# Performance work log

Hardware: AMD Instinct MI355X
Metric: run time of the kernel (lower is better)

Reference implementation:

```python
import jax, jax.numpy as jnp
import numpy as np

VOCAB, E, HID, HD, S, T = 50000, 1024, 1024, 512, 4096, 20
START, STOP, NEG = 18, 19, -10000.0


def setup_inputs() -> dict:
    key = jax.random.key(0)
    ks = jax.random.split(key, 16)
    scale = 0.05
    trans = jax.random.normal(ks[12], (T, T), jnp.float32)
    trans = trans.at[START, :].set(NEG).at[:, START].set(NEG)
    return {
        'sentence': jax.random.randint(ks[0], (S,), 0, VOCAB),
        'embed_table': jax.random.normal(ks[1], (VOCAB, E), jnp.float32) * scale,
        'w_ih_f': jax.random.normal(ks[2], (4 * HD, E), jnp.float32) * scale,
        'w_hh_f': jax.random.normal(ks[3], (4 * HD, HD), jnp.float32) * scale,
        'b_ih_f': jax.random.normal(ks[4], (4 * HD,), jnp.float32) * scale,
        'b_hh_f': jax.random.normal(ks[5], (4 * HD,), jnp.float32) * scale,
        'w_ih_b': jax.random.normal(ks[6], (4 * HD, E), jnp.float32) * scale,
        'w_hh_b': jax.random.normal(ks[7], (4 * HD, HD), jnp.float32) * scale,
        'b_ih_b': jax.random.normal(ks[8], (4 * HD,), jnp.float32) * scale,
        'b_hh_b': jax.random.normal(ks[9], (4 * HD,), jnp.float32) * scale,
        'w_out': jax.random.normal(ks[10], (T, HID), jnp.float32) * scale,
        'b_out': jax.random.normal(ks[11], (T,), jnp.float32) * scale,
        'transitions': trans,
        'h0': jax.random.normal(ks[13], (2, HD), jnp.float32),
        'c0': jax.random.normal(ks[14], (2, HD), jnp.float32),
    }


def _lstm_dir(pre, w_hh, b_hh, h0, c0, reverse):
    # pre: [S, 4HD] = x @ W_ih^T + b_ih (precomputed big GEMM)
    def step(carry, p):
        h, c = carry
        g = p + h @ w_hh.T + b_hh
        i, f, gg, o = jnp.split(g, 4, axis=-1)  # torch gate order i,f,g,o
        c = jax.nn.sigmoid(f) * c + jax.nn.sigmoid(i) * jnp.tanh(gg)
        h = jax.nn.sigmoid(o) * jnp.tanh(c)
        return (h, c), h
    _, hs = jax.lax.scan(step, (h0, c0), pre, reverse=reverse)
    return hs  # [S, HD], time-aligned in both directions


def _get_feats(sentence, embed_table, w_ih_f, w_hh_f, b_ih_f, b_hh_f,
               w_ih_b, w_hh_b, b_ih_b, b_hh_b, w_out, b_out, h0, c0):
    x = embed_table[sentence]                       # [S, E]
    hf = _lstm_dir(x @ w_ih_f.T + b_ih_f, w_hh_f, b_hh_f, h0[0], c0[0], False)
    hb = _lstm_dir(x @ w_ih_b.T + b_ih_b, w_hh_b, b_hh_b, h0[1], c0[1], True)
    lstm_out = jnp.concatenate([hf, hb], axis=-1)   # [S, HID]
    return lstm_out @ w_out.T + b_out               # [S, T]


def reference(sentence, embed_table, w_ih_f, w_hh_f, b_ih_f, b_hh_f,
              w_ih_b, w_hh_b, b_ih_b, b_hh_b, w_out, b_out,
              transitions, h0, c0):
    feats = _get_feats(sentence, embed_table, w_ih_f, w_hh_f, b_ih_f, b_hh_f,
                       w_ih_b, w_hh_b, b_ih_b, b_hh_b, w_out, b_out, h0, c0)
    # Viterbi decode
    init_v = jnp.full((T,), NEG, jnp.float32).at[START].set(0.0)

    def step(fv, feat):
        nt = fv[None, :] + transitions            # [T_cur, T_prev]
        best = jnp.argmax(nt, axis=1)             # backpointers [T]
        fv_new = jnp.max(nt, axis=1) + feat
        return fv_new, best

    fv_last, bptrs = jax.lax.scan(step, init_v, feats)
    terminal = fv_last + transitions[STOP]
    path_score = jnp.max(terminal)
    best_tag = jnp.argmax(terminal)

    def back(tag, bp):
        return bp[tag], tag
    _, path = jax.lax.scan(back, best_tag, bptrs, reverse=True)  # [S]
    return path_score, path
```

## Files before the change

### kernel.cpp

```cpp
#include <hip/hip_runtime.h>
#include <math.h>

#define S_LEN 4096
#define NTAG 20
#define TAG_STOP 19
#define NEGV -10000.0f
#define NWG 16


__global__ void init_ws(unsigned long long* hpub) {
    int i = blockIdx.x * 256 + threadIdx.x;
    if (i < 2048) hpub[i] = 0ull;
}

__device__ __forceinline__ float sigm(float x) { return 1.0f / (1.0f + expf(-x)); }

__launch_bounds__(256)
__global__ void pre_gemm(const int* __restrict__ sent, const float* __restrict__ embed,
                         const float* __restrict__ wf, const float* __restrict__ wb,
                         const float* __restrict__ bihf, const float* __restrict__ bhhf,
                         const float* __restrict__ bihb, const float* __restrict__ bhhb,
                         float* __restrict__ pre)
{
    __shared__ float As[16][68];
    __shared__ float Bs[16][136];
    __shared__ int   srow[64];
    const int tid = threadIdx.x;
    const int bm = blockIdx.x & 63;
    const int bn = blockIdx.x >> 6;
    const int pos0 = bm * 64, row0 = bn * 128;
    if (tid < 64) srow[tid] = sent[pos0 + tid];
    __syncthreads();

    const int tx = tid & 15, ty = tid >> 4;
    float acc[4][8];
    #pragma unroll
    for (int m = 0; m < 4; ++m)
        #pragma unroll
        for (int n = 0; n < 8; ++n) acc[m][n] = 0.f;

    for (int kt = 0; kt < 1024; kt += 16) {
        {
            int m = tid >> 2, kc = (tid & 3) * 4;
            const float* src = embed + (size_t)srow[m] * 1024 + kt + kc;
            float4 v = *(const float4*)src;
            As[kc+0][m] = v.x; As[kc+1][m] = v.y; As[kc+2][m] = v.z; As[kc+3][m] = v.w;
        }
        #pragma unroll
        for (int it = 0; it < 2; ++it) {
            int n = (tid >> 2) + it * 64;
            int kc = (tid & 3) * 4;
            int grow = row0 + n;
            const float* wsrc = (grow < 2048) ? (wf + (size_t)grow * 1024)
                                              : (wb + (size_t)(grow - 2048) * 1024);
            float4 v = *(const float4*)(wsrc + kt + kc);
            Bs[kc+0][n] = v.x; Bs[kc+1][n] = v.y; Bs[kc+2][n] = v.z; Bs[kc+3][n] = v.w;
        }
        __syncthreads();
        #pragma unroll
        for (int kk = 0; kk < 16; ++kk) {
            float a[4], b[8];
            float4 av = *(const float4*)&As[kk][ty * 4];
            a[0] = av.x; a[1] = av.y; a[2] = av.z; a[3] = av.w;
            float4 bv0 = *(const float4*)&Bs[kk][tx * 8];
            float4 bv1 = *(const float4*)&Bs[kk][tx * 8 + 4];
            b[0]=bv0.x; b[1]=bv0.y; b[2]=bv0.z; b[3]=bv0.w;
            b[4]=bv1.x; b[5]=bv1.y; b[6]=bv1.z; b[7]=bv1.w;
            #pragma unroll
            for (int m = 0; m < 4; ++m)
                #pragma unroll
                for (int n = 0; n < 8; ++n) acc[m][n] += a[m] * b[n];
        }
        __syncthreads();
    }
    #pragma unroll
    for (int m = 0; m < 4; ++m) {
        int pos = pos0 + ty * 4 + m;
        #pragma unroll
        for (int n = 0; n < 8; ++n) {
            int grow = row0 + tx * 8 + n;
            float bias = (grow < 2048) ? (bihf[grow] + bhhf[grow])
                                       : (bihb[grow - 2048] + bhhb[grow - 2048]);
            pre[(size_t)pos * 4096 + grow] = acc[m][n] + bias;
        }
    }
}

template<int P>
__device__ __forceinline__ void lstm_step(
    int s, int dir, int wg, int j, int ks, int su, bool own, int sidx, bool gate,
    const float* __restrict__ pre, const float* __restrict__ h0,
    float* __restrict__ hs, unsigned long long* pub,
    float (&buf)[2][576],
    const float (&wr0)[32], const float (&wr1)[32],
    const float (&wr2)[32], const float (&wr3)[32],
    float (&pf)[4], float& c_reg)
{
    if (s == 0) {
        buf[0][sidx] = h0[dir * 512 + su];
    } else if (!own) {
        const unsigned int expect = (unsigned int)s;
        unsigned long long u = __hip_atomic_load(&pub[P * 512 + su],
                                                 __ATOMIC_RELAXED, __HIP_MEMORY_SCOPE_AGENT);
        while ((unsigned int)(u >> 32) < expect)
            u = __hip_atomic_load(&pub[P * 512 + su],
                                  __ATOMIC_RELAXED, __HIP_MEMORY_SCOPE_AGENT);
        buf[P][sidx] = __uint_as_float((unsigned int)u);
    }
    __syncthreads();

    float a0 = 0.f, a1 = 0.f, a2 = 0.f, a3 = 0.f;
    const float* hp = &buf[P][ks * 36];
    #pragma unroll
    for (int q = 0; q < 8; ++q) {
        float4 h4 = ((const float4*)hp)[q];
        a0 += wr0[q*4+0]*h4.x + wr0[q*4+1]*h4.y + wr0[q*4+2]*h4.z + wr0[q*4+3]*h4.w;
        a1 += wr1[q*4+0]*h4.x + wr1[q*4+1]*h4.y + wr1[q*4+2]*h4.z + wr1[q*4+3]*h4.w;
        a2 += wr2[q*4+0]*h4.x + wr2[q*4+1]*h4.y + wr2[q*4+2]*h4.z + wr2[q*4+3]*h4.w;
        a3 += wr3[q*4+0]*h4.x + wr3[q*4+1]*h4.y + wr3[q*4+2]*h4.z + wr3[q*4+3]*h4.w;
    }
    a0 += __shfl_xor(a0, 1); a0 += __shfl_xor(a0, 2); a0 += __shfl_xor(a0, 4); a0 += __shfl_xor(a0, 8);
    a1 += __shfl_xor(a1, 1); a1 += __shfl_xor(a1, 2); a1 += __shfl_xor(a1, 4); a1 += __shfl_xor(a1, 8);
    a2 += __shfl_xor(a2, 1); a2 += __shfl_xor(a2, 2); a2 += __shfl_xor(a2, 4); a2 += __shfl_xor(a2, 8);
    a3 += __shfl_xor(a3, 1); a3 += __shfl_xor(a3, 2); a3 += __shfl_xor(a3, 4); a3 += __shfl_xor(a3, 8);

    if (gate) {
        float gi = a0 + pf[0], gf = a1 + pf[1], gg = a2 + pf[2], go = a3 + pf[3];
        float cn = sigm(gf) * c_reg + sigm(gi) * tanhf(gg);
        float hN = sigm(go) * tanhf(cn);
        c_reg = cn;
        const int pos = dir ? (S_LEN - 1 - s) : s;
        hs[((size_t)dir * S_LEN + pos) * 512 + j] = hN;
        buf[P ^ 1][j + 4 * wg] = hN;
        unsigned long long uv = ((unsigned long long)(unsigned int)(s + 1) << 32)
                              | (unsigned long long)__float_as_uint(hN);
        __hip_atomic_store(&pub[(P ^ 1) * 512 + j], uv,
                           __ATOMIC_RELAXED, __HIP_MEMORY_SCOPE_AGENT);
        if (s + 2 < S_LEN) {
            const int pp = dir ? (S_LEN - 3 - s) : (s + 2);
            const float* pb = pre + (size_t)pp * 4096 + dir * 2048 + j;
            pf[0] = pb[0]; pf[1] = pb[512]; pf[2] = pb[1024]; pf[3] = pb[1536];
        }
    }
}

__launch_bounds__(512, 2)
__global__ void lstm_kernel(const float* __restrict__ pre,
                            const float* __restrict__ w_hh_f, const float* __restrict__ w_hh_b,
                            const float* __restrict__ h0, const float* __restrict__ c0,
                            float* __restrict__ hs, unsigned long long* __restrict__ h_pub)
{
    const int dir  = blockIdx.x >> 4;
    const int wg   = blockIdx.x & 15;
    const int tid  = threadIdx.x;
    const int wv   = tid >> 6;
    const int lane = tid & 63;
    const int rg   = lane >> 4;
    const int ks   = lane & 15;
    const int j    = wg * 32 + wv * 4 + rg;
    const float* w_hh = dir ? w_hh_b : w_hh_f;

    __shared__ float buf[2][576];

    float wr0[32], wr1[32], wr2[32], wr3[32];
    {
        const float* wbase = w_hh + (size_t)j * 512 + ks * 32;
        #pragma unroll
        for (int q = 0; q < 8; ++q) {
            float4 v0 = *(const float4*)(wbase + 0 * 262144 + q * 4);
            wr0[q*4+0] = v0.x; wr0[q*4+1] = v0.y; wr0[q*4+2] = v0.z; wr0[q*4+3] = v0.w;
            float4 v1 = *(const float4*)(wbase + 1 * 262144 + q * 4);
            wr1[q*4+0] = v1.x; wr1[q*4+1] = v1.y; wr1[q*4+2] = v1.z; wr1[q*4+3] = v1.w;
            float4 v2 = *(const float4*)(wbase + 2 * 262144 + q * 4);
            wr2[q*4+0] = v2.x; wr2[q*4+1] = v2.y; wr2[q*4+2] = v2.z; wr2[q*4+3] = v2.w;
            float4 v3 = *(const float4*)(wbase + 3 * 262144 + q * 4);
            wr3[q*4+0] = v3.x; wr3[q*4+1] = v3.y; wr3[q*4+2] = v3.z; wr3[q*4+3] = v3.w;
        }
    }

    const bool gate = (ks == 0);
    float c_reg = 0.f;
    float pfA[4] = {0,0,0,0}, pfB[4] = {0,0,0,0};
    if (gate) {
        c_reg = c0[dir * 512 + j];
        const int p0 = dir ? (S_LEN - 1) : 0;
        const int p1 = dir ? (S_LEN - 2) : 1;
        const float* b0 = pre + (size_t)p0 * 4096 + dir * 2048 + j;
        const float* b1 = pre + (size_t)p1 * 4096 + dir * 2048 + j;
        pfA[0] = b0[0]; pfA[1] = b0[512]; pfA[2] = b0[1024]; pfA[3] = b0[1536];
        pfB[0] = b1[0]; pfB[1] = b1[512]; pfB[2] = b1[1024]; pfB[3] = b1[1536];
    }

    const int  su   = tid;
    const bool own  = ((su >> 5) == wg);
    const int  sidx = su + ((su >> 5) << 2);
    unsigned long long* pub = h_pub + dir * 1024;

    for (int s = 0; s < S_LEN; s += 2) {
        lstm_step<0>(s,     dir, wg, j, ks, su, own, sidx, gate,
                     pre, h0, hs, pub, buf, wr0, wr1, wr2, wr3, pfA, c_reg);
        lstm_step<1>(s + 1, dir, wg, j, ks, su, own, sidx, gate,
                     pre, h0, hs, pub, buf, wr0, wr1, wr2, wr3, pfB, c_reg);
    }
}

__launch_bounds__(256)
__global__ void feats_kernel(const float* __restrict__ hs, const float* __restrict__ w_out,
                             const float* __restrict__ b_out, float* __restrict__ feats)
{
    const int pos = blockIdx.x;
    const int tid = threadIdx.x;
    __shared__ float hbuf[1024];
    __shared__ float red[160];
    {
        const float* hf = hs + (size_t)pos * 512;
        const float* hb = hs + ((size_t)S_LEN + pos) * 512;
        if (tid < 128) *(float4*)&hbuf[tid * 4]           = *(const float4*)&hf[tid * 4];
        else           *(float4*)&hbuf[512 + (tid-128)*4] = *(const float4*)&hb[(tid - 128) * 4];
    }
    __syncthreads();
    if (tid < 160) {
        int tag = tid >> 3, part = tid & 7;
        const float* wrow = w_out + (size_t)tag * 1024 + part * 128;
        const float* hrow = hbuf + part * 128;
        float sum = 0.f;
        #pragma unroll
        for (int q = 0; q < 32; ++q) {
            float4 a = ((const float4*)hrow)[q];
            float4 b = ((const float4*)wrow)[q];
            sum += a.x*b.x + a.y*b.y + a.z*b.z + a.w*b.w;
        }
        red[tid] = sum;
    }
    __syncthreads();
    if (tid < NTAG) {
        float sum = b_out[tid];
        #pragma unroll
        for (int p = 0; p < 8; ++p) sum += red[tid * 8 + p];
        feats[(size_t)pos * NTAG + tid] = sum;
    }
}

__launch_bounds__(256)
__global__ void viterbi_kernel(const float* __restrict__ feats, const float* __restrict__ trans,
                               unsigned char* __restrict__ bptr, float* __restrict__ out)
{
    __shared__ float feat_lds[64 * NTAG];
    __shared__ int sh_best;
    __shared__ unsigned char Mmap[8][NTAG];
    __shared__ unsigned char entry_s[8];
    const int tid = threadIdx.x;

    if (tid < 64) {
        const int lane = tid;
        const int i = (lane < NTAG) ? lane : (NTAG - 1);
        float trow[NTAG];
        #pragma unroll
        for (int jj = 0; jj < NTAG; ++jj) trow[jj] = trans[i * NTAG + jj];
        float fv[NTAG];
        #pragma unroll
        for (int jj = 0; jj < NTAG; ++jj) fv[jj] = (jj == 18) ? 0.f : NEGV;

        for (int blk = 0; blk < 64; ++blk) {
            #pragma unroll
            for (int q = 0; q < 20; ++q)
                feat_lds[q * 64 + lane] = feats[blk * 1280 + q * 64 + lane];
            for (int ss = 0; ss < 64; ++ss) {
                int s = blk * 64 + ss;
                float best = fv[0] + trow[0];
                int bj = 0;
                #pragma unroll
                for (int jj = 1; jj < NTAG; ++jj) {
                    float cand = fv[jj] + trow[jj];
                    if (cand > best) { best = cand; bj = jj; }
                }
                float fnew = best + feat_lds[ss * NTAG + i];
                if (lane < NTAG) bptr[s * NTAG + lane] = (unsigned char)bj;
                #pragma unroll
                for (int jj = 0; jj < NTAG; ++jj) fv[jj] = __shfl(fnew, jj);
            }
        }
        if (lane == 0) {
            float best = -1e30f; int bt = 0;
            for (int jj = 0; jj < NTAG; ++jj) {
                float t2 = fv[jj] + trans[TAG_STOP * NTAG + jj];
                if (t2 > best) { best = t2; bt = jj; }
            }
            out[0] = best;
            sh_best = bt;
        }
    }
    __syncthreads();
    if (tid < 160) {
        int c = tid / NTAG, e = tid % NTAG;
        int tag = e;
        for (int t = (c + 1) * 512 - 1; t >= c * 512; --t) tag = bptr[t * NTAG + tag];
        Mmap[c][e] = (unsigned char)tag;
    }
    __syncthreads();
    if (tid == 0) {
        int e = sh_best;
        entry_s[7] = (unsigned char)e;
        for (int c = 7; c >= 1; --c) { e = Mmap[c][e]; entry_s[c - 1] = (unsigned char)e; }
    }
    __syncthreads();
    if (tid < 8) {
        int c = tid;
        int tag = entry_s[c];
        out[1 + (c + 1) * 512 - 1] = (float)tag;
        for (int t = (c + 1) * 512 - 1; t > c * 512; --t) {
            tag = bptr[t * NTAG + tag];
            out[1 + t - 1] = (float)tag;
        }
    }
}

extern "C" void kernel_launch(void* const* d_in, const int* in_sizes, int n_in,
                              void* d_out, int out_size, void* d_ws, size_t ws_size,
                              hipStream_t stream) {
    (void)in_sizes; (void)n_in; (void)out_size; (void)ws_size;
    const int*   sent  = (const int*)d_in[0];
    const float* embed = (const float*)d_in[1];
    const float* wihf  = (const float*)d_in[2];
    const float* whhf  = (const float*)d_in[3];
    const float* bihf  = (const float*)d_in[4];
    const float* bhhf  = (const float*)d_in[5];
    const float* wihb  = (const float*)d_in[6];
    const float* whhb  = (const float*)d_in[7];
    const float* bihb  = (const float*)d_in[8];
    const float* bhhb  = (const float*)d_in[9];
    const float* wout  = (const float*)d_in[10];
    const float* bout  = (const float*)d_in[11];
    const float* trans = (const float*)d_in[12];
    const float* h0    = (const float*)d_in[13];
    const float* c0    = (const float*)d_in[14];

    char* ws = (char*)d_ws;
    unsigned long long* h_pub = (unsigned long long*)(ws + 4096);
    float* pre   = (float*)(ws + 65536);
    float* hs    = (float*)(ws + 65536 + (size_t)4096 * 4096 * 4);
    float* feats = (float*)(ws + 65536 + (size_t)4096 * 4096 * 4 + (size_t)2 * 4096 * 512 * 4);
    unsigned char* bptr = (unsigned char*)(feats + (size_t)S_LEN * NTAG);
    float* out = (float*)d_out;

    hipLaunchKernelGGL(init_ws, dim3(8), dim3(256), 0, stream, h_pub);
    hipLaunchKernelGGL(pre_gemm, dim3(2048), dim3(256), 0, stream,
                       sent, embed, wihf, wihb, bihf, bhhf, bihb, bhhb, pre);
    hipLaunchKernelGGL(lstm_kernel, dim3(32), dim3(512), 0, stream,
                       pre, whhf, whhb, h0, c0, hs, h_pub);
    hipLaunchKernelGGL(feats_kernel, dim3(S_LEN), dim3(256), 0, stream,
                       hs, wout, bout, feats);
    hipLaunchKernelGGL(viterbi_kernel, dim3(1), dim3(256), 0, stream,
                       feats, trans, bptr, out);
}
```

Measured before the change: 10.70 ms.

## Split LSTM recurrent gate rows across two half-groups with 1024-thread blocks

The recurrent LSTM kernel now runs 1024 threads per workgroup instead of 512. Each hidden unit is served by 32 lanes, and each 16-lane half computes two of the four gate dot products, cutting per-thread weight registers from 128 to 64 and halving the serial FMA chain per step. The halves exchange partial sums with a shuffle. The gate lane in one half publishes h to global memory while the other half writes hs and the shared buffer, and polling is spread across 8 lanes per unit. The cost is more threads per workgroup and barrier participants, plus an extra cross-half shuffle on each step.

```diff
diff --git a/kernel.cpp b/kernel.cpp
--- a/kernel.cpp
+++ b/kernel.cpp
@@ -5,7 +5,6 @@
 #define NTAG 20
 #define TAG_STOP 19
 #define NEGV -10000.0f
-#define NWG 16
 
 
 __global__ void init_ws(unsigned long long* hpub) {
@@ -88,54 +87,57 @@
 
 template<int P>
 __device__ __forceinline__ void lstm_step(
-    int s, int dir, int wg, int j, int ks, int su, bool own, int sidx, bool gate,
+    int s, int dir, int wg, int j, int hf, int ks,
+    bool isPoller, int p, bool own, int sidx, bool glane,
     const float* __restrict__ pre, const float* __restrict__ h0,
     float* __restrict__ hs, unsigned long long* pub,
     float (&buf)[2][576],
     const float (&wr0)[32], const float (&wr1)[32],
-    const float (&wr2)[32], const float (&wr3)[32],
     float (&pf)[4], float& c_reg)
 {
     if (s == 0) {
-        buf[0][sidx] = h0[dir * 512 + su];
-    } else if (!own) {
+        if (isPoller) buf[0][sidx] = h0[dir * 512 + p];
+    } else if (isPoller && !own) {
         const unsigned int expect = (unsigned int)s;
-        unsigned long long u = __hip_atomic_load(&pub[P * 512 + su],
+        unsigned long long u = __hip_atomic_load(&pub[P * 512 + p],
                                                  __ATOMIC_RELAXED, __HIP_MEMORY_SCOPE_AGENT);
         while ((unsigned int)(u >> 32) < expect)
-            u = __hip_atomic_load(&pub[P * 512 + su],
+            u = __hip_atomic_load(&pub[P * 512 + p],
                                   __ATOMIC_RELAXED, __HIP_MEMORY_SCOPE_AGENT);
         buf[P][sidx] = __uint_as_float((unsigned int)u);
     }
     __syncthreads();
 
-    float a0 = 0.f, a1 = 0.f, a2 = 0.f, a3 = 0.f;
+    float a0 = 0.f, a1 = 0.f;
     const float* hp = &buf[P][ks * 36];
     #pragma unroll
     for (int q = 0; q < 8; ++q) {
         float4 h4 = ((const float4*)hp)[q];
         a0 += wr0[q*4+0]*h4.x + wr0[q*4+1]*h4.y + wr0[q*4+2]*h4.z + wr0[q*4+3]*h4.w;
         a1 += wr1[q*4+0]*h4.x + wr1[q*4+1]*h4.y + wr1[q*4+2]*h4.z + wr1[q*4+3]*h4.w;
-        a2 += wr2[q*4+0]*h4.x + wr2[q*4+1]*h4.y + wr2[q*4+2]*h4.z + wr2[q*4+3]*h4.w;
-        a3 += wr3[q*4+0]*h4.x + wr3[q*4+1]*h4.y + wr3[q*4+2]*h4.z + wr3[q*4+3]*h4.w;
     }
     a0 += __shfl_xor(a0, 1); a0 += __shfl_xor(a0, 2); a0 += __shfl_xor(a0, 4); a0 += __shfl_xor(a0, 8);
     a1 += __shfl_xor(a1, 1); a1 += __shfl_xor(a1, 2); a1 += __shfl_xor(a1, 4); a1 += __shfl_xor(a1, 8);
-    a2 += __shfl_xor(a2, 1); a2 += __shfl_xor(a2, 2); a2 += __shfl_xor(a2, 4); a2 += __shfl_xor(a2, 8);
-    a3 += __shfl_xor(a3, 1); a3 += __shfl_xor(a3, 2); a3 += __shfl_xor(a3, 4); a3 += __shfl_xor(a3, 8);
-
-    if (gate) {
-        float gi = a0 + pf[0], gf = a1 + pf[1], gg = a2 + pf[2], go = a3 + pf[3];
+    float b0 = __shfl_xor(a0, 16);
+    float b1 = __shfl_xor(a1, 16);
+
+    if (glane) {
+        float gi, gf, gg, go;
+        if (hf == 0) { gi = a0 + pf[0]; gf = a1 + pf[1]; gg = b0 + pf[2]; go = b1 + pf[3]; }
+        else         { gi = b0 + pf[0]; gf = b1 + pf[1]; gg = a0 + pf[2]; go = a1 + pf[3]; }
         float cn = sigm(gf) * c_reg + sigm(gi) * tanhf(gg);
         float hN = sigm(go) * tanhf(cn);
         c_reg = cn;
-        const int pos = dir ? (S_LEN - 1 - s) : s;
-        hs[((size_t)dir * S_LEN + pos) * 512 + j] = hN;
-        buf[P ^ 1][j + 4 * wg] = hN;
-        unsigned long long uv = ((unsigned long long)(unsigned int)(s + 1) << 32)
-                              | (unsigned long long)__float_as_uint(hN);
-        __hip_atomic_store(&pub[(P ^ 1) * 512 + j], uv,
-                           __ATOMIC_RELAXED, __HIP_MEMORY_SCOPE_AGENT);
+        if (hf == 0) {
+            unsigned long long uv = ((unsigned long long)(unsigned int)(s + 1) << 32)
+                                  | (unsigned long long)__float_as_uint(hN);
+            __hip_atomic_store(&pub[(P ^ 1) * 512 + j], uv,
+                               __ATOMIC_RELAXED, __HIP_MEMORY_SCOPE_AGENT);
+        } else {
+            const int pos = dir ? (S_LEN - 1 - s) : s;
+            hs[((size_t)dir * S_LEN + pos) * 512 + j] = hN;
+            buf[P ^ 1][j + 4 * wg] = hN;
+        }
         if (s + 2 < S_LEN) {
             const int pp = dir ? (S_LEN - 3 - s) : (s + 2);
             const float* pb = pre + (size_t)pp * 4096 + dir * 2048 + j;
@@ -144,7 +146,7 @@
     }
 }
 
-__launch_bounds__(512, 2)
+__launch_bounds__(1024, 4)
 __global__ void lstm_kernel(const float* __restrict__ pre,
                             const float* __restrict__ w_hh_f, const float* __restrict__ w_hh_b,
                             const float* __restrict__ h0, const float* __restrict__ c0,
@@ -153,35 +155,30 @@
     const int dir  = blockIdx.x >> 4;
     const int wg   = blockIdx.x & 15;
     const int tid  = threadIdx.x;
-    const int wv   = tid >> 6;
-    const int lane = tid & 63;
-    const int rg   = lane >> 4;
-    const int ks   = lane & 15;
-    const int j    = wg * 32 + wv * 4 + rg;
+    const int g    = tid >> 5;
+    const int hf   = (tid >> 4) & 1;
+    const int ks   = tid & 15;
+    const int j    = wg * 32 + g;
     const float* w_hh = dir ? w_hh_b : w_hh_f;
 
     __shared__ float buf[2][576];
 
-    float wr0[32], wr1[32], wr2[32], wr3[32];
+    float wr0[32], wr1[32];
     {
-        const float* wbase = w_hh + (size_t)j * 512 + ks * 32;
+        const float* wbase = w_hh + ((size_t)(hf * 2) * 512 + j) * 512 + ks * 32;
         #pragma unroll
         for (int q = 0; q < 8; ++q) {
-            float4 v0 = *(const float4*)(wbase + 0 * 262144 + q * 4);
+            float4 v0 = *(const float4*)(wbase + q * 4);
             wr0[q*4+0] = v0.x; wr0[q*4+1] = v0.y; wr0[q*4+2] = v0.z; wr0[q*4+3] = v0.w;
-            float4 v1 = *(const float4*)(wbase + 1 * 262144 + q * 4);
+            float4 v1 = *(const float4*)(wbase + 262144 + q * 4);
             wr1[q*4+0] = v1.x; wr1[q*4+1] = v1.y; wr1[q*4+2] = v1.z; wr1[q*4+3] = v1.w;
-            float4 v2 = *(const float4*)(wbase + 2 * 262144 + q * 4);
-            wr2[q*4+0] = v2.x; wr2[q*4+1] = v2.y; wr2[q*4+2] = v2.z; wr2[q*4+3] = v2.w;
-            float4 v3 = *(const float4*)(wbase + 3 * 262144 + q * 4);
-            wr3[q*4+0] = v3.x; wr3[q*4+1] = v3.y; wr3[q*4+2] = v3.z; wr3[q*4+3] = v3.w;
-        }
-    }
-
-    const bool gate = (ks == 0);
+        }
+    }
+
+    const bool glane = (ks == 0);
     float c_reg = 0.f;
     float pfA[4] = {0,0,0,0}, pfB[4] = {0,0,0,0};
-    if (gate) {
+    if (glane) {
         c_reg = c0[dir * 512 + j];
         const int p0 = dir ? (S_LEN - 1) : 0;
         const int p1 = dir ? (S_LEN - 2) : 1;
@@ -191,16 +188,18 @@
         pfB[0] = b1[0]; pfB[1] = b1[512]; pfB[2] = b1[1024]; pfB[3] = b1[1536];
     }
 
-    const int  su   = tid;
-    const bool own  = ((su >> 5) == wg);
-    const int  sidx = su + ((su >> 5) << 2);
+    const int  ksm      = ks - 1;
+    const bool isPoller = (ksm >= 0 && ksm < 8);
+    const int  p        = g * 16 + hf * 8 + (ksm & 7);
+    const bool own      = ((p >> 5) == wg);
+    const int  sidx     = p + ((p >> 5) << 2);
     unsigned long long* pub = h_pub + dir * 1024;
 
     for (int s = 0; s < S_LEN; s += 2) {
-        lstm_step<0>(s,     dir, wg, j, ks, su, own, sidx, gate,
-                     pre, h0, hs, pub, buf, wr0, wr1, wr2, wr3, pfA, c_reg);
-        lstm_step<1>(s + 1, dir, wg, j, ks, su, own, sidx, gate,
-                     pre, h0, hs, pub, buf, wr0, wr1, wr2, wr3, pfB, c_reg);
+        lstm_step<0>(s,     dir, wg, j, hf, ks, isPoller, p, own, sidx, glane,
+                     pre, h0, hs, pub, buf, wr0, wr1, pfA, c_reg);
+        lstm_step<1>(s + 1, dir, wg, j, hf, ks, isPoller, p, own, sidx, glane,
+                     pre, h0, hs, pub, buf, wr0, wr1, pfB, c_reg);
     }
 }
 
@@ -236,7 +235,7 @@
     if (tid < NTAG) {
         float sum = b_out[tid];
         #pragma unroll
-        for (int p = 0; p < 8; ++p) sum += red[tid * 8 + p];
+        for (int pq = 0; pq < 8; ++pq) sum += red[tid * 8 + pq];
         feats[(size_t)pos * NTAG + tid] = sum;
     }
 }
@@ -346,7 +345,7 @@
     hipLaunchKernelGGL(init_ws, dim3(8), dim3(256), 0, stream, h_pub);
     hipLaunchKernelGGL(pre_gemm, dim3(2048), dim3(256), 0, stream,
                        sent, embed, wihf, wihb, bihf, bhhf, bihb, bhhb, pre);
-    hipLaunchKernelGGL(lstm_kernel, dim3(32), dim3(512), 0, stream,
+    hipLaunchKernelGGL(lstm_kernel, dim3(32), dim3(1024), 0, stream,
                        pre, whhf, whhb, h0, c0, hs, h_pub);
     hipLaunchKernelGGL(feats_kernel, dim3(S_LEN), dim3(256), 0, stream,
                        hs, wout, bout, feats);
```

Result: slower. 11.56 ms (+8.1%).
